# Performance work log

Measured on AMD Instinct MI355X. Metric: run time of the kernel, lower is better.

## Reference

```python
import jax, jax.numpy as jnp
import numpy as np

N, E, D_IN, D_H = 20000, 320000, 512, 512
ALPHA = 0.1
LAMBDA = 1.0

def setup_inputs() -> dict:
    key = jax.random.key(0)
    ks = jax.random.split(key, 12)
    feat = jax.random.normal(ks[0], (N, D_IN), dtype=jnp.float32)
    src = jax.random.randint(ks[1], (E,), 0, N, dtype=jnp.int32)
    dst = jax.random.randint(ks[2], (E,), 0, N, dtype=jnp.int32)
    s = 0.05
    fc_w = jax.random.normal(ks[3], (D_H, D_IN), dtype=jnp.float32) * s  # torch Linear: [out,in]
    fc_b = jax.random.normal(ks[4], (D_H,), dtype=jnp.float32) * s
    w1_1 = jax.random.normal(ks[5], (D_H, D_H), dtype=jnp.float32) * s
    w2_1 = jax.random.normal(ks[6], (D_H, D_H), dtype=jnp.float32) * s
    b_1 = jax.random.normal(ks[7], (D_H,), dtype=jnp.float32) * s
    w1_2 = jax.random.normal(ks[8], (D_H, D_H), dtype=jnp.float32) * s
    w2_2 = jax.random.normal(ks[9], (D_H, D_H), dtype=jnp.float32) * s
    b_2 = jax.random.normal(ks[10], (D_H,), dtype=jnp.float32) * s
    return {"feat": feat, "src": src, "dst": dst, "fc_w": fc_w, "fc_b": fc_b,
            "w1_1": w1_1, "w2_1": w2_1, "b_1": b_1,
            "w1_2": w1_2, "w2_2": w2_2, "b_2": b_2}


def _gcn2_layer(h, h0, src, dst, norm, w1, w2, b, layer):
    # DGL GCN2Conv (project_initial_features=False)
    beta = float(np.log(LAMBDA / layer + 1.0))
    x = h * norm                      # [N, D]
    agg = jax.ops.segment_sum(x[src], dst, num_segments=h.shape[0])  # SpMM: sum over in-neighbors
    agg = agg * norm
    f = agg * (1.0 - ALPHA)
    f0 = h0 * ALPHA
    rst = ((1.0 - beta) * f + beta * (f @ w1)
           + (1.0 - beta) * f0 + beta * (f0 @ w2) + b)
    return jax.nn.relu(rst)


def reference(feat, src, dst, fc_w, fc_b, w1_1, w2_1, b_1, w1_2, w2_2, b_2):
    n = feat.shape[0]
    h = feat @ fc_w.T + fc_b          # initial projection
    # symmetric norm from in-degrees (clamped at 1), as in DGL
    deg = jax.ops.segment_sum(jnp.ones_like(dst, dtype=h.dtype), dst, num_segments=n)
    norm = jnp.clip(deg, 1.0, None) ** -0.5
    norm = norm[:, None]
    res = _gcn2_layer(h, h, src, dst, norm, w1_1, w2_1, b_1, layer=1)
    out = _gcn2_layer(res, h, src, dst, norm, w1_2, w2_2, b_2, layer=2)
    return out
```

## Files before the change

kernel.cpp:

```cpp
#include <hip/hip_runtime.h>
#include <hip/hip_bf16.h>
#include <stdint.h>
#include <stddef.h>

typedef __bf16 bf16_t;
typedef __bf16 bf16x4 __attribute__((ext_vector_type(4)));
typedef __bf16 bf16x8 __attribute__((ext_vector_type(8)));
typedef float floatx4 __attribute__((ext_vector_type(4)));

#define NN 20000
#define EE 320000
#define DD 512
#define CAP 96
#define BETA1 0.6931471805599453f
#define BETA2 0.40546510810816444f

__device__ __forceinline__ void gload16(const bf16_t* g, bf16_t* l) {
  __builtin_amdgcn_global_load_lds((const __attribute__((address_space(1))) uint32_t*)g,
                                   (__attribute__((address_space(3))) uint32_t*)l, 16, 0, 0);
}

__global__ __launch_bounds__(256) void bucket_kernel(
    const int* __restrict__ src, const int* __restrict__ dst,
    int* __restrict__ cnt, int* __restrict__ esrc, int E) {
  int e = blockIdx.x * 256 + threadIdx.x;
  if (e < E) {
    int d = dst[e];
    int pos = atomicAdd(&cnt[d], 1);
    if (pos < CAP) esrc[d * CAP + pos] = src[e];
  }
}

#define PREP_BLOCKS 5719
__global__ __launch_bounds__(256) void prep_kernel(
    const float* __restrict__ feat, const float* __restrict__ fc_w,
    const float* __restrict__ w1_1, const float* __restrict__ w2_1,
    const float* __restrict__ w1_2, const float* __restrict__ w2_2,
    bf16_t* __restrict__ featb, bf16_t* __restrict__ bw0,
    bf16_t* __restrict__ bt1, bf16_t* __restrict__ bt2,
    int* __restrict__ cnt) {
  int b = blockIdx.x, t = threadIdx.x;
  if (b < 5128) {
    const float* in = (b < 5000) ? feat : fc_w;
    bf16_t* out = (b < 5000) ? featb : bw0;
    size_t c = (size_t)(b < 5000 ? b : b - 5000) * 256 + t;
    const float* s = in + c * 8;
    float4 v0 = *(const float4*)s, v1 = *(const float4*)(s + 4);
    bf16x8 o = {(bf16_t)v0.x, (bf16_t)v0.y, (bf16_t)v0.z, (bf16_t)v0.w,
                (bf16_t)v1.x, (bf16_t)v1.y, (bf16_t)v1.z, (bf16_t)v1.w};
    *(bf16x8*)(out + c * 8) = o;
  } else if (b < 5640) {
    int base = (b < 5384) ? 5128 : 5384;
    const float* Wa = (b < 5384) ? w1_1 : w1_2;
    const float* Wb = (b < 5384) ? w2_1 : w2_2;
    bf16_t* bt = (b < 5384) ? bt1 : bt2;
    int c = (b - base) * 256 + t;
    int n = c >> 7, kc = c & 127;
    const float* W = (kc < 64) ? Wa : Wb;
    int kcw = kc & 63;
    bf16x8 o;
#pragma unroll
    for (int e = 0; e < 8; ++e)
      o[e] = (bf16_t)W[(size_t)(kcw * 8 + e) * 512 + n];
    *(bf16x8*)(bt + (size_t)n * 1024 + kc * 8) = o;
  } else {
    int i = (b - 5640) * 256 + t;
    if (i < NN) cnt[i] = 0;
  }
}

__global__ __launch_bounds__(256) void aggregate_kernel(
    const bf16_t* __restrict__ hin, const float* __restrict__ nrm,
    const int* __restrict__ cnt, const int* __restrict__ esrc,
    bf16_t* __restrict__ Acat) {
  int node = blockIdx.x * 4 + (threadIdx.x >> 6);
  if (node >= NN) return;
  int lane = threadIdx.x & 63;
  const int* eb = esrc + (size_t)node * CAP;
  int n_e = cnt[node];
  n_e = n_e < CAP ? n_e : CAP;

  float acc[8] = {};
  bf16x8 v0 = {}, v1 = {}, v2 = {}, v3 = {}, v4 = {}, v5 = {}, v6 = {}, v7 = {};
  float ns0 = 0, ns1 = 0, ns2 = 0, ns3 = 0, ns4 = 0, ns5 = 0, ns6 = 0, ns7 = 0;

#define LOADJ(j, idx)                                                  \
  {                                                                    \
    int s = eb[idx];                                                   \
    ns##j = nrm[s];                                                    \
    v##j = *(const bf16x8*)(hin + (size_t)s * DD + lane * 8);          \
  }
#define SLOT(j, i)                                                     \
  if ((i) + (j) < n_e) {                                               \
    bf16x8 a = v##j; float na = ns##j;                                 \
    if ((i) + (j) + 8 < n_e) LOADJ(j, (i) + (j) + 8)                   \
    _Pragma("unroll")                                                  \
    for (int k = 0; k < 8; ++k) acc[k] += na * (float)a[k];            \
  }

  if (0 < n_e) LOADJ(0, 0)
  if (1 < n_e) LOADJ(1, 1)
  if (2 < n_e) LOADJ(2, 2)
  if (3 < n_e) LOADJ(3, 3)
  if (4 < n_e) LOADJ(4, 4)
  if (5 < n_e) LOADJ(5, 5)
  if (6 < n_e) LOADJ(6, 6)
  if (7 < n_e) LOADJ(7, 7)

  for (int i = 0; i < n_e; i += 8) {
    SLOT(0, i)
    SLOT(1, i)
    SLOT(2, i)
    SLOT(3, i)
    SLOT(4, i)
    SLOT(5, i)
    SLOT(6, i)
    SLOT(7, i)
  }
#undef SLOT
#undef LOADJ

  float nd = 0.9f * nrm[node];
  bf16x8 ob;
#pragma unroll
  for (int k = 0; k < 8; ++k) ob[k] = (bf16_t)(nd * acc[k]);
  *(bf16x8*)(Acat + (size_t)node * 1024 + lane * 8) = ob;
}

template <int MODE>
__global__ __launch_bounds__(256) void gemm_kernel(
    const bf16_t* __restrict__ A, const bf16_t* __restrict__ BT,
    int lda, int ldb, int K, int M,
    const float* __restrict__ bias,
    const bf16_t* __restrict__ acat_ro, float beta,
    float* __restrict__ outf, bf16_t* __restrict__ outb,
    bf16_t* __restrict__ acat2,
    const int* __restrict__ cnt, float* __restrict__ nrm) {
  __shared__ bf16_t As[2][64 * 64];
  __shared__ bf16_t Bs[2][128 * 64];

  const int bid = blockIdx.x;
  if constexpr (MODE == 0) {
    if (bid >= 1280) {
      int i = (bid - 1280) * 256 + threadIdx.x;
      if (i < NN) nrm[i] = 1.0f / sqrtf(fmaxf((float)cnt[i], 1.0f));
      return;
    }
  }
  const int mt = (bid >> 5) * 8 + (bid & 7);
  const int nt = (bid >> 3) & 3;
  const int m0 = mt * 64;
  if (m0 >= M) return;
  const int n0 = nt * 128;

  const int t = threadIdx.x;
  const int lane = t & 63;
  const int w = t >> 6;
  const int wm = w & 1, wn = w >> 1;
  const int quad = lane >> 4, m16 = lane & 15;

  const int tr = t >> 3;
  const int gc = (t & 7) ^ (tr & 7);
  int arow0 = m0 + tr;      arow0 = arow0 < M ? arow0 : M - 1;
  int arow1 = m0 + tr + 32; arow1 = arow1 < M ? arow1 : M - 1;
  const bf16_t* agp0 = A + (size_t)arow0 * lda + gc * 8;
  const bf16_t* agp1 = A + (size_t)arow1 * lda + gc * 8;
  const bf16_t* bgp0 = BT + (size_t)(n0 + tr) * ldb + gc * 8;
  const bf16_t* bgp1 = BT + (size_t)(n0 + tr + 32) * ldb + gc * 8;
  const bf16_t* bgp2 = BT + (size_t)(n0 + tr + 64) * ldb + gc * 8;
  const bf16_t* bgp3 = BT + (size_t)(n0 + tr + 96) * ldb + gc * 8;

#define STAGE(buf, ko)                              \
  gload16(agp0 + (ko), &As[buf][t * 8]);            \
  gload16(agp1 + (ko), &As[buf][(t + 256) * 8]);    \
  gload16(bgp0 + (ko), &Bs[buf][t * 8]);            \
  gload16(bgp1 + (ko), &Bs[buf][(t + 256) * 8]);    \
  gload16(bgp2 + (ko), &Bs[buf][(t + 512) * 8]);    \
  gload16(bgp3 + (ko), &Bs[buf][(t + 768) * 8]);

  floatx4 acc[2][4] = {};
  const int niter = K >> 6;

  STAGE(0, 0)

  for (int kt = 0; kt < niter; ++kt) {
    __syncthreads();
    const int b = kt & 1;
    if (kt + 1 < niter) {
      const int ko = (kt + 1) * 64;
      STAGE(b ^ 1, ko)
    }

#pragma unroll
    for (int ks = 0; ks < 2; ++ks) {
      bf16x8 af[2], bfr[4];
#pragma unroll
      for (int i = 0; i < 2; ++i) {
        int arow = wm * 32 + i * 16 + m16;
        int cc = (ks * 4 + quad) ^ (arow & 7);
        af[i] = *(const bf16x8*)(&As[b][(arow * 8 + cc) * 8]);
      }
#pragma unroll
      for (int j = 0; j < 4; ++j) {
        int brow = wn * 64 + j * 16 + m16;
        int cc = (ks * 4 + quad) ^ (brow & 7);
        bfr[j] = *(const bf16x8*)(&Bs[b][(brow * 8 + cc) * 8]);
      }
#pragma unroll
      for (int i = 0; i < 2; ++i)
#pragma unroll
        for (int j = 0; j < 4; ++j)
          acc[i][j] = __builtin_amdgcn_mfma_f32_16x16x32_bf16(af[i], bfr[j], acc[i][j], 0, 0, 0);
    }
  }
#undef STAGE

#pragma unroll
  for (int i = 0; i < 2; ++i) {
#pragma unroll
    for (int j = 0; j < 4; ++j) {
      int col = n0 + wn * 64 + j * 16 + m16;
      float bv = bias[col];
#pragma unroll
      for (int p = 0; p < 4; ++p) {
        int row = m0 + wm * 32 + i * 16 + quad * 4 + p;
        if (row < M) {
          size_t idx = (size_t)row * DD + col;
          float v = acc[i][j][p];
          if constexpr (MODE == 0) {
            float hv = v + bv;
            outb[idx] = (bf16_t)hv;
            acat2[(size_t)row * 1024 + 512 + col] = (bf16_t)(0.1f * hv);
          } else {
            float fsv = (float)acat_ro[(size_t)row * 1024 + col] +
                        (float)acat_ro[(size_t)row * 1024 + 512 + col];
            float r = (1.0f - beta) * fsv + beta * v + bv;
            r = fmaxf(r, 0.0f);
            if constexpr (MODE == 1) outb[idx] = (bf16_t)r;
            else outf[idx] = r;
          }
        }
      }
    }
  }
}

extern "C" void kernel_launch(void* const* d_in, const int* in_sizes, int n_in,
                              void* d_out, int out_size, void* d_ws, size_t ws_size,
                              hipStream_t stream) {
  const float* feat = (const float*)d_in[0];
  const int* src = (const int*)d_in[1];
  const int* dst = (const int*)d_in[2];
  const float* fc_w = (const float*)d_in[3];
  const float* fc_b = (const float*)d_in[4];
  const float* w1_1 = (const float*)d_in[5];
  const float* w2_1 = (const float*)d_in[6];
  const float* b_1  = (const float*)d_in[7];
  const float* w1_2 = (const float*)d_in[8];
  const float* w2_2 = (const float*)d_in[9];
  const float* b_2  = (const float*)d_in[10];
  float* out = (float*)d_out;

  char* ws = (char*)d_ws;
  size_t off = 0;
  auto alloc = [&](size_t bytes) {
    char* p = ws + off;
    off += (bytes + 255) & ~(size_t)255;
    return p;
  };
  const size_t NDf = (size_t)NN * DD;
  bf16_t* h_bf   = (bf16_t*)alloc(NDf * sizeof(bf16_t));
  bf16_t* res_bf = (bf16_t*)alloc(NDf * sizeof(bf16_t));
  bf16_t* featb  = (bf16_t*)alloc(NDf * sizeof(bf16_t));
  bf16_t* Acat   = (bf16_t*)alloc((size_t)NN * 1024 * sizeof(bf16_t));
  bf16_t* BW0    = (bf16_t*)alloc((size_t)512 * 512 * sizeof(bf16_t));
  bf16_t* BT1    = (bf16_t*)alloc((size_t)512 * 1024 * sizeof(bf16_t));
  bf16_t* BT2    = (bf16_t*)alloc((size_t)512 * 1024 * sizeof(bf16_t));
  int*    cnt    = (int*)alloc((size_t)NN * sizeof(int));
  float*  nrm    = (float*)alloc((size_t)NN * sizeof(float));
  int*    esrc   = (int*)alloc((size_t)NN * CAP * sizeof(int));

  prep_kernel<<<PREP_BLOCKS, 256, 0, stream>>>(feat, fc_w, w1_1, w2_1, w1_2, w2_2,
                                               featb, BW0, BT1, BT2, cnt);
  bucket_kernel<<<(EE + 255) / 256, 256, 0, stream>>>(src, dst, cnt, esrc, EE);

  gemm_kernel<0><<<1280 + 79, 256, 0, stream>>>(featb, BW0, 512, 512, 512, NN, fc_b,
                                                nullptr, 0.0f, nullptr, h_bf, Acat,
                                                cnt, nrm);

  aggregate_kernel<<<(NN + 3) / 4, 256, 0, stream>>>(h_bf, nrm, cnt, esrc, Acat);
  gemm_kernel<1><<<1280, 256, 0, stream>>>(Acat, BT1, 1024, 1024, 1024, NN, b_1,
                                           Acat, BETA1, nullptr, res_bf, nullptr,
                                           nullptr, nullptr);

  aggregate_kernel<<<(NN + 3) / 4, 256, 0, stream>>>(res_bf, nrm, cnt, esrc, Acat);
  gemm_kernel<2><<<1280, 256, 0, stream>>>(Acat, BT2, 1024, 1024, 1024, NN, b_2,
                                           Acat, BETA2, out, nullptr, nullptr,
                                           nullptr, nullptr);
}
```

Before: 360.7 us.

## Use triple-buffered K=32 LDS pipeline with explicit vmcnt waits in GEMM

Changes the GEMM mainloop from a double-buffered 64-wide K tile to a triple-buffered 32-wide K tile, with two stages in flight. Each iteration waits with s_waitcnt vmcnt(3) instead of a full __syncthreads drain, and the LDS layout and swizzle are adjusted to the narrower rows. The goal is to hide global-load latency better and keep LDS usage similar. The cost is twice as many barriers per K and less MFMA work between them.

Measured after the change: 381.4 us. 1.06x slower.

```diff
diff --git a/kernel.cpp b/kernel.cpp
--- a/kernel.cpp
+++ b/kernel.cpp
@@ -136,8 +136,8 @@
     float* __restrict__ outf, bf16_t* __restrict__ outb,
     bf16_t* __restrict__ acat2,
     const int* __restrict__ cnt, float* __restrict__ nrm) {
-  __shared__ bf16_t As[2][64 * 64];
-  __shared__ bf16_t Bs[2][128 * 64];
+  __shared__ bf16_t As[3][64 * 32];
+  __shared__ bf16_t Bs[3][128 * 32];
 
   const int bid = blockIdx.x;
   if constexpr (MODE == 0) {
@@ -159,61 +159,71 @@
   const int wm = w & 1, wn = w >> 1;
   const int quad = lane >> 4, m16 = lane & 15;
 
-  const int tr = t >> 3;
-  const int gc = (t & 7) ^ (tr & 7);
-  int arow0 = m0 + tr;      arow0 = arow0 < M ? arow0 : M - 1;
-  int arow1 = m0 + tr + 32; arow1 = arow1 < M ? arow1 : M - 1;
-  const bf16_t* agp0 = A + (size_t)arow0 * lda + gc * 8;
-  const bf16_t* agp1 = A + (size_t)arow1 * lda + gc * 8;
-  const bf16_t* bgp0 = BT + (size_t)(n0 + tr) * ldb + gc * 8;
-  const bf16_t* bgp1 = BT + (size_t)(n0 + tr + 32) * ldb + gc * 8;
-  const bf16_t* bgp2 = BT + (size_t)(n0 + tr + 64) * ldb + gc * 8;
-  const bf16_t* bgp3 = BT + (size_t)(n0 + tr + 96) * ldb + gc * 8;
+  const int hi = t >> 3;
+  const int z = (t & 7) ^ (hi & 7);
+  const int ra = hi * 2 + (z >> 2);
+  const int gc = z & 3;
+  int arow = m0 + ra; arow = arow < M ? arow : M - 1;
+  const bf16_t* agp  = A + (size_t)arow * lda + gc * 8;
+  const bf16_t* bgp0 = BT + (size_t)(n0 + ra) * ldb + gc * 8;
+  const bf16_t* bgp1 = BT + (size_t)(n0 + 64 + ra) * ldb + gc * 8;
 
 #define STAGE(buf, ko)                              \
-  gload16(agp0 + (ko), &As[buf][t * 8]);            \
-  gload16(agp1 + (ko), &As[buf][(t + 256) * 8]);    \
+  gload16(agp + (ko),  &As[buf][t * 8]);            \
   gload16(bgp0 + (ko), &Bs[buf][t * 8]);            \
-  gload16(bgp1 + (ko), &Bs[buf][(t + 256) * 8]);    \
-  gload16(bgp2 + (ko), &Bs[buf][(t + 512) * 8]);    \
-  gload16(bgp3 + (ko), &Bs[buf][(t + 768) * 8]);
+  gload16(bgp1 + (ko), &Bs[buf][(t + 256) * 8]);
+
+#define COMPUTE(b)                                                               \
+  {                                                                              \
+    bf16x8 af[2], bfr[4];                                                        \
+    _Pragma("unroll")                                                            \
+    for (int i = 0; i < 2; ++i) {                                                \
+      int ar = wm * 32 + i * 16 + m16;                                           \
+      int s8 = (((ar & 1) << 2) | quad) ^ ((ar >> 1) & 7);                       \
+      af[i] = *(const bf16x8*)(&As[b][((ar >> 1) * 8 + s8) * 8]);                \
+    }                                                                            \
+    _Pragma("unroll")                                                            \
+    for (int j = 0; j < 4; ++j) {                                                \
+      int br = wn * 64 + j * 16 + m16;                                           \
+      int s8 = (((br & 1) << 2) | quad) ^ ((br >> 1) & 7);                       \
+      bfr[j] = *(const bf16x8*)(&Bs[b][((br >> 1) * 8 + s8) * 8]);               \
+    }                                                                            \
+    _Pragma("unroll")                                                            \
+    for (int i = 0; i < 2; ++i)                                                  \
+      _Pragma("unroll")                                                          \
+      for (int j = 0; j < 4; ++j)                                                \
+        acc[i][j] = __builtin_amdgcn_mfma_f32_16x16x32_bf16(af[i], bfr[j],       \
+                                                            acc[i][j], 0, 0, 0); \
+  }
 
   floatx4 acc[2][4] = {};
-  const int niter = K >> 6;
+  const int niter = K >> 5;
 
   STAGE(0, 0)
-
-  for (int kt = 0; kt < niter; ++kt) {
-    __syncthreads();
-    const int b = kt & 1;
-    if (kt + 1 < niter) {
-      const int ko = (kt + 1) * 64;
-      STAGE(b ^ 1, ko)
+  STAGE(1, 32)
+
+  int cur = 0, nx = 2;
+  for (int kt = 0; kt < niter - 1; ++kt) {
+    asm volatile("s_waitcnt vmcnt(3)" ::: "memory");
+    asm volatile("s_waitcnt lgkmcnt(0)" ::: "memory");
+    __builtin_amdgcn_s_barrier();
+    __builtin_amdgcn_sched_barrier(0);
+    if (kt + 2 < niter) {
+      const int ko = (kt + 2) * 32;
+      STAGE(nx, ko)
     }
-
-#pragma unroll
-    for (int ks = 0; ks < 2; ++ks) {
-      bf16x8 af[2], bfr[4];
-#pragma unroll
-      for (int i = 0; i < 2; ++i) {
-        int arow = wm * 32 + i * 16 + m16;
-        int cc = (ks * 4 + quad) ^ (arow & 7);
-        af[i] = *(const bf16x8*)(&As[b][(arow * 8 + cc) * 8]);
-      }
-#pragma unroll
-      for (int j = 0; j < 4; ++j) {
-        int brow = wn * 64 + j * 16 + m16;
-        int cc = (ks * 4 + quad) ^ (brow & 7);
-        bfr[j] = *(const bf16x8*)(&Bs[b][(brow * 8 + cc) * 8]);
-      }
-#pragma unroll
-      for (int i = 0; i < 2; ++i)
-#pragma unroll
-        for (int j = 0; j < 4; ++j)
-          acc[i][j] = __builtin_amdgcn_mfma_f32_16x16x32_bf16(af[i], bfr[j], acc[i][j], 0, 0, 0);
-    }
-  }
+    COMPUTE(cur)
+    cur = (cur == 2) ? 0 : cur + 1;
+    nx = (nx == 2) ? 0 : nx + 1;
+  }
+  asm volatile("s_waitcnt vmcnt(0)" ::: "memory");
+  asm volatile("s_waitcnt lgkmcnt(0)" ::: "memory");
+  __builtin_amdgcn_s_barrier();
+  __builtin_amdgcn_sched_barrier(0);
+  COMPUTE(cur)
+
 #undef STAGE
+#undef COMPUTE
 
 #pragma unroll
   for (int i = 0; i < 2; ++i) {
```

## Store unscaled h once in Acat and aggregate two nodes per wavefront

Applied to the files above, without the earlier changes.

The first GEMM now writes the unscaled projection h only into the second half of Acat, instead of writing both a separate h buffer and a 0.1-scaled copy. The 0.1 factor is folded into the W2 weight conversion and the epilogue, and the first aggregation reads h from Acat with a stride of 1024. The aggregation kernel also handles two destination nodes per wavefront, each with 4 in-flight loads, so more independent gathers are outstanding at once. The aim is to cut a full N×512 bf16 write and shorten gather latency, at the cost of strided reads and uneven work when the two nodes have different degrees.

After: 370.5 us. 2.7% more time.

```diff
diff --git a/kernel.cpp b/kernel.cpp
--- a/kernel.cpp
+++ b/kernel.cpp
@@ -57,11 +57,12 @@
     int c = (b - base) * 256 + t;
     int n = c >> 7, kc = c & 127;
     const float* W = (kc < 64) ? Wa : Wb;
+    const float sc = (kc < 64) ? 1.0f : 0.1f;
     int kcw = kc & 63;
     bf16x8 o;
 #pragma unroll
     for (int e = 0; e < 8; ++e)
-      o[e] = (bf16_t)W[(size_t)(kcw * 8 + e) * 512 + n];
+      o[e] = (bf16_t)(sc * W[(size_t)(kcw * 8 + e) * 512 + n]);
     *(bf16x8*)(bt + (size_t)n * 1024 + kc * 8) = o;
   } else {
     int i = (b - 5640) * 256 + t;
@@ -70,61 +71,86 @@
 }
 
 __global__ __launch_bounds__(256) void aggregate_kernel(
-    const bf16_t* __restrict__ hin, const float* __restrict__ nrm,
+    const bf16_t* __restrict__ hin, int hstride, const float* __restrict__ nrm,
     const int* __restrict__ cnt, const int* __restrict__ esrc,
     bf16_t* __restrict__ Acat) {
-  int node = blockIdx.x * 4 + (threadIdx.x >> 6);
-  if (node >= NN) return;
+  int nodeA = blockIdx.x * 8 + (threadIdx.x >> 6) * 2;
+  int nodeB = nodeA + 1;
+  if (nodeA >= NN) return;
   int lane = threadIdx.x & 63;
-  const int* eb = esrc + (size_t)node * CAP;
-  int n_e = cnt[node];
-  n_e = n_e < CAP ? n_e : CAP;
-
-  float acc[8] = {};
-  bf16x8 v0 = {}, v1 = {}, v2 = {}, v3 = {}, v4 = {}, v5 = {}, v6 = {}, v7 = {};
-  float ns0 = 0, ns1 = 0, ns2 = 0, ns3 = 0, ns4 = 0, ns5 = 0, ns6 = 0, ns7 = 0;
-
-#define LOADJ(j, idx)                                                  \
-  {                                                                    \
-    int s = eb[idx];                                                   \
-    ns##j = nrm[s];                                                    \
-    v##j = *(const bf16x8*)(hin + (size_t)s * DD + lane * 8);          \
-  }
-#define SLOT(j, i)                                                     \
-  if ((i) + (j) < n_e) {                                               \
-    bf16x8 a = v##j; float na = ns##j;                                 \
-    if ((i) + (j) + 8 < n_e) LOADJ(j, (i) + (j) + 8)                   \
-    _Pragma("unroll")                                                  \
-    for (int k = 0; k < 8; ++k) acc[k] += na * (float)a[k];            \
-  }
-
-  if (0 < n_e) LOADJ(0, 0)
-  if (1 < n_e) LOADJ(1, 1)
-  if (2 < n_e) LOADJ(2, 2)
-  if (3 < n_e) LOADJ(3, 3)
-  if (4 < n_e) LOADJ(4, 4)
-  if (5 < n_e) LOADJ(5, 5)
-  if (6 < n_e) LOADJ(6, 6)
-  if (7 < n_e) LOADJ(7, 7)
-
-  for (int i = 0; i < n_e; i += 8) {
-    SLOT(0, i)
-    SLOT(1, i)
-    SLOT(2, i)
-    SLOT(3, i)
-    SLOT(4, i)
-    SLOT(5, i)
-    SLOT(6, i)
-    SLOT(7, i)
-  }
-#undef SLOT
-#undef LOADJ
-
-  float nd = 0.9f * nrm[node];
-  bf16x8 ob;
-#pragma unroll
-  for (int k = 0; k < 8; ++k) ob[k] = (bf16_t)(nd * acc[k]);
-  *(bf16x8*)(Acat + (size_t)node * 1024 + lane * 8) = ob;
+  const int* ebA = esrc + (size_t)nodeA * CAP;
+  const int* ebB = esrc + (size_t)nodeB * CAP;
+  int nA = cnt[nodeA]; nA = nA < CAP ? nA : CAP;
+  int nB = cnt[nodeB]; nB = nB < CAP ? nB : CAP;
+  int nmax = nA > nB ? nA : nB;
+
+  float accA[8] = {}, accB[8] = {};
+  bf16x8 va0 = {}, va1 = {}, va2 = {}, va3 = {};
+  bf16x8 vb0 = {}, vb1 = {}, vb2 = {}, vb3 = {};
+  float sa0 = 0, sa1 = 0, sa2 = 0, sa3 = 0;
+  float sb0 = 0, sb1 = 0, sb2 = 0, sb3 = 0;
+
+#define LDA(j, idx)                                                      \
+  {                                                                      \
+    int s = ebA[idx];                                                    \
+    sa##j = nrm[s];                                                      \
+    va##j = *(const bf16x8*)(hin + (size_t)s * hstride + lane * 8);      \
+  }
+#define LDB(j, idx)                                                      \
+  {                                                                      \
+    int s = ebB[idx];                                                    \
+    sb##j = nrm[s];                                                      \
+    vb##j = *(const bf16x8*)(hin + (size_t)s * hstride + lane * 8);      \
+  }
+#define SLA(j, i)                                                        \
+  if ((i) + (j) < nA) {                                                  \
+    bf16x8 a = va##j; float na = sa##j;                                  \
+    if ((i) + (j) + 4 < nA) LDA(j, (i) + (j) + 4)                        \
+    _Pragma("unroll")                                                    \
+    for (int k = 0; k < 8; ++k) accA[k] += na * (float)a[k];             \
+  }
+#define SLB(j, i)                                                        \
+  if ((i) + (j) < nB) {                                                  \
+    bf16x8 a = vb##j; float na = sb##j;                                  \
+    if ((i) + (j) + 4 < nB) LDB(j, (i) + (j) + 4)                        \
+    _Pragma("unroll")                                                    \
+    for (int k = 0; k < 8; ++k) accB[k] += na * (float)a[k];             \
+  }
+
+  if (0 < nA) LDA(0, 0)
+  if (0 < nB) LDB(0, 0)
+  if (1 < nA) LDA(1, 1)
+  if (1 < nB) LDB(1, 1)
+  if (2 < nA) LDA(2, 2)
+  if (2 < nB) LDB(2, 2)
+  if (3 < nA) LDA(3, 3)
+  if (3 < nB) LDB(3, 3)
+
+  for (int i = 0; i < nmax; i += 4) {
+    SLA(0, i)
+    SLB(0, i)
+    SLA(1, i)
+    SLB(1, i)
+    SLA(2, i)
+    SLB(2, i)
+    SLA(3, i)
+    SLB(3, i)
+  }
+#undef SLA
+#undef SLB
+#undef LDA
+#undef LDB
+
+  float ndA = 0.9f * nrm[nodeA];
+  float ndB = 0.9f * nrm[nodeB];
+  bf16x8 oA, oB;
+#pragma unroll
+  for (int k = 0; k < 8; ++k) {
+    oA[k] = (bf16_t)(ndA * accA[k]);
+    oB[k] = (bf16_t)(ndB * accB[k]);
+  }
+  *(bf16x8*)(Acat + (size_t)nodeA * 1024 + lane * 8) = oA;
+  *(bf16x8*)(Acat + (size_t)nodeB * 1024 + lane * 8) = oB;
 }
 
 template <int MODE>
@@ -225,15 +251,13 @@
       for (int p = 0; p < 4; ++p) {
         int row = m0 + wm * 32 + i * 16 + quad * 4 + p;
         if (row < M) {
-          size_t idx = (size_t)row * DD + col;
           float v = acc[i][j][p];
           if constexpr (MODE == 0) {
-            float hv = v + bv;
-            outb[idx] = (bf16_t)hv;
-            acat2[(size_t)row * 1024 + 512 + col] = (bf16_t)(0.1f * hv);
+            acat2[(size_t)row * 1024 + 512 + col] = (bf16_t)(v + bv);
           } else {
+            size_t idx = (size_t)row * DD + col;
             float fsv = (float)acat_ro[(size_t)row * 1024 + col] +
-                        (float)acat_ro[(size_t)row * 1024 + 512 + col];
+                        0.1f * (float)acat_ro[(size_t)row * 1024 + 512 + col];
             float r = (1.0f - beta) * fsv + beta * v + bv;
             r = fmaxf(r, 0.0f);
             if constexpr (MODE == 1) outb[idx] = (bf16_t)r;
@@ -269,7 +293,6 @@
     return p;
   };
   const size_t NDf = (size_t)NN * DD;
-  bf16_t* h_bf   = (bf16_t*)alloc(NDf * sizeof(bf16_t));
   bf16_t* res_bf = (bf16_t*)alloc(NDf * sizeof(bf16_t));
   bf16_t* featb  = (bf16_t*)alloc(NDf * sizeof(bf16_t));
   bf16_t* Acat   = (bf16_t*)alloc((size_t)NN * 1024 * sizeof(bf16_t));
@@ -285,15 +308,15 @@
   bucket_kernel<<<(EE + 255) / 256, 256, 0, stream>>>(src, dst, cnt, esrc, EE);
 
   gemm_kernel<0><<<1280 + 79, 256, 0, stream>>>(featb, BW0, 512, 512, 512, NN, fc_b,
-                                                nullptr, 0.0f, nullptr, h_bf, Acat,
+                                                nullptr, 0.0f, nullptr, nullptr, Acat,
                                                 cnt, nrm);
 
-  aggregate_kernel<<<(NN + 3) / 4, 256, 0, stream>>>(h_bf, nrm, cnt, esrc, Acat);
+  aggregate_kernel<<<NN / 8, 256, 0, stream>>>(Acat + 512, 1024, nrm, cnt, esrc, Acat);
   gemm_kernel<1><<<1280, 256, 0, stream>>>(Acat, BT1, 1024, 1024, 1024, NN, b_1,
                                            Acat, BETA1, nullptr, res_bf, nullptr,
                                            nullptr, nullptr);
 
-  aggregate_kernel<<<(NN + 3) / 4, 256, 0, stream>>>(res_bf, nrm, cnt, esrc, Acat);
+  aggregate_kernel<<<NN / 8, 256, 0, stream>>>(res_bf, 512, nrm, cnt, esrc, Acat);
   gemm_kernel<2><<<1280, 256, 0, stream>>>(Acat, BT2, 1024, 1024, 1024, NN, b_2,
                                            Acat, BETA2, out, nullptr, nullptr,
                                            nullptr, nullptr);
```

## Pre-scale features by source norm and pipeline aggregation gathers through LDS

Applied to the files above, without the earlier changes.

The GEMM epilogues now write features already multiplied by the source-node norm (computed inline from degree counts), so the aggregation no longer loads a per-edge norm and the separate norm array and pass are removed. The 0.1 alpha factor moves into the W2 weights and the epilogue. The aggregation kernel is rewritten to load edge indices four at a time and gather neighbor rows asynchronously into a double-buffered LDS ring using global_load_lds with explicit vmcnt waits. To keep the fixed-size chunk index loads safe, the prep kernel zero-fills the edge bucket buffer, which adds extra write traffic.

New measurement: 342.6 us. 1.05x faster.

```diff
diff --git a/kernel.cpp b/kernel.cpp
--- a/kernel.cpp
+++ b/kernel.cpp
@@ -31,14 +31,14 @@
   }
 }
 
-#define PREP_BLOCKS 5719
+#define PREP_BLOCKS 7594
 __global__ __launch_bounds__(256) void prep_kernel(
     const float* __restrict__ feat, const float* __restrict__ fc_w,
     const float* __restrict__ w1_1, const float* __restrict__ w2_1,
     const float* __restrict__ w1_2, const float* __restrict__ w2_2,
     bf16_t* __restrict__ featb, bf16_t* __restrict__ bw0,
     bf16_t* __restrict__ bt1, bf16_t* __restrict__ bt2,
-    int* __restrict__ cnt) {
+    int* __restrict__ cnt, int* __restrict__ esrc) {
   int b = blockIdx.x, t = threadIdx.x;
   if (b < 5128) {
     const float* in = (b < 5000) ? feat : fc_w;
@@ -57,70 +57,89 @@
     int c = (b - base) * 256 + t;
     int n = c >> 7, kc = c & 127;
     const float* W = (kc < 64) ? Wa : Wb;
+    const float sc = (kc < 64) ? 1.0f : 0.1f;
     int kcw = kc & 63;
     bf16x8 o;
 #pragma unroll
     for (int e = 0; e < 8; ++e)
-      o[e] = (bf16_t)W[(size_t)(kcw * 8 + e) * 512 + n];
+      o[e] = (bf16_t)(sc * W[(size_t)(kcw * 8 + e) * 512 + n]);
     *(bf16x8*)(bt + (size_t)n * 1024 + kc * 8) = o;
-  } else {
+  } else if (b < 5719) {
     int i = (b - 5640) * 256 + t;
     if (i < NN) cnt[i] = 0;
+  } else {
+    int i = (b - 5719) * 256 + t;
+    ((int4*)esrc)[i] = make_int4(0, 0, 0, 0);
   }
 }
 
 __global__ __launch_bounds__(256) void aggregate_kernel(
-    const bf16_t* __restrict__ hin, const float* __restrict__ nrm,
-    const int* __restrict__ cnt, const int* __restrict__ esrc,
-    bf16_t* __restrict__ Acat) {
-  int node = blockIdx.x * 4 + (threadIdx.x >> 6);
-  if (node >= NN) return;
-  int lane = threadIdx.x & 63;
+    const bf16_t* __restrict__ hs, const int* __restrict__ cnt,
+    const int* __restrict__ esrc, bf16_t* __restrict__ Acat) {
+  __shared__ bf16_t ring[4][2][4][512];
+  const int w = threadIdx.x >> 6;
+  const int lane = threadIdx.x & 63;
+  const int node = blockIdx.x * 4 + w;
   const int* eb = esrc + (size_t)node * CAP;
-  int n_e = cnt[node];
-  n_e = n_e < CAP ? n_e : CAP;
+  int ncnt = cnt[node];
+  int n_e = ncnt < CAP ? ncnt : CAP;
+  float nd = 0.9f * rsqrtf(fmaxf((float)ncnt, 1.0f));
+  int nchunks = (n_e + 3) >> 2;
 
   float acc[8] = {};
-  bf16x8 v0 = {}, v1 = {}, v2 = {}, v3 = {}, v4 = {}, v5 = {}, v6 = {}, v7 = {};
-  float ns0 = 0, ns1 = 0, ns2 = 0, ns3 = 0, ns4 = 0, ns5 = 0, ns6 = 0, ns7 = 0;
-
-#define LOADJ(j, idx)                                                  \
-  {                                                                    \
-    int s = eb[idx];                                                   \
-    ns##j = nrm[s];                                                    \
-    v##j = *(const bf16x8*)(hin + (size_t)s * DD + lane * 8);          \
-  }
-#define SLOT(j, i)                                                     \
-  if ((i) + (j) < n_e) {                                               \
-    bf16x8 a = v##j; float na = ns##j;                                 \
-    if ((i) + (j) + 8 < n_e) LOADJ(j, (i) + (j) + 8)                   \
-    _Pragma("unroll")                                                  \
-    for (int k = 0; k < 8; ++k) acc[k] += na * (float)a[k];            \
-  }
-
-  if (0 < n_e) LOADJ(0, 0)
-  if (1 < n_e) LOADJ(1, 1)
-  if (2 < n_e) LOADJ(2, 2)
-  if (3 < n_e) LOADJ(3, 3)
-  if (4 < n_e) LOADJ(4, 4)
-  if (5 < n_e) LOADJ(5, 5)
-  if (6 < n_e) LOADJ(6, 6)
-  if (7 < n_e) LOADJ(7, 7)
-
-  for (int i = 0; i < n_e; i += 8) {
-    SLOT(0, i)
-    SLOT(1, i)
-    SLOT(2, i)
-    SLOT(3, i)
-    SLOT(4, i)
-    SLOT(5, i)
-    SLOT(6, i)
-    SLOT(7, i)
-  }
-#undef SLOT
-#undef LOADJ
-
-  float nd = 0.9f * nrm[node];
+  bf16_t* r0base = &ring[w][0][0][lane * 8];
+  bf16_t* r1base = &ring[w][1][0][lane * 8];
+
+  int4 icur, inext;
+
+  asm volatile("s_waitcnt vmcnt(0)" ::: "memory");
+  __builtin_amdgcn_sched_barrier(0);
+  icur = *(const int4*)(eb);
+  asm volatile("s_waitcnt vmcnt(0)" ::: "memory");
+  __builtin_amdgcn_sched_barrier(0);
+  inext = *(const int4*)(eb + 4);
+  gload16(hs + (size_t)icur.x * DD + lane * 8, r0base);
+  gload16(hs + (size_t)icur.y * DD + lane * 8, r0base + 512);
+  gload16(hs + (size_t)icur.z * DD + lane * 8, r0base + 1024);
+  gload16(hs + (size_t)icur.w * DD + lane * 8, r0base + 1536);
+
+  for (int c = 0; c < nchunks; ++c) {
+    asm volatile("s_waitcnt vmcnt(4)" ::: "memory");
+    __builtin_amdgcn_sched_barrier(0);
+    int4 iuse = inext;
+    int off2 = (c + 2) * 4; off2 = off2 > CAP - 4 ? CAP - 4 : off2;
+    inext = *(const int4*)(eb + off2);
+    bf16_t* rbn = ((c + 1) & 1) ? r1base : r0base;
+    gload16(hs + (size_t)iuse.x * DD + lane * 8, rbn);
+    gload16(hs + (size_t)iuse.y * DD + lane * 8, rbn + 512);
+    gload16(hs + (size_t)iuse.z * DD + lane * 8, rbn + 1024);
+    gload16(hs + (size_t)iuse.w * DD + lane * 8, rbn + 1536);
+    asm volatile("s_waitcnt vmcnt(5)" ::: "memory");
+    __builtin_amdgcn_sched_barrier(0);
+    bf16_t* rb = (c & 1) ? r1base : r0base;
+    bf16x8 v0 = *(const bf16x8*)(rb);
+    bf16x8 v1 = *(const bf16x8*)(rb + 512);
+    bf16x8 v2 = *(const bf16x8*)(rb + 1024);
+    bf16x8 v3 = *(const bf16x8*)(rb + 1536);
+    int e0 = c * 4;
+    if (e0 < n_e) {
+#pragma unroll
+      for (int k = 0; k < 8; ++k) acc[k] += (float)v0[k];
+    }
+    if (e0 + 1 < n_e) {
+#pragma unroll
+      for (int k = 0; k < 8; ++k) acc[k] += (float)v1[k];
+    }
+    if (e0 + 2 < n_e) {
+#pragma unroll
+      for (int k = 0; k < 8; ++k) acc[k] += (float)v2[k];
+    }
+    if (e0 + 3 < n_e) {
+#pragma unroll
+      for (int k = 0; k < 8; ++k) acc[k] += (float)v3[k];
+    }
+  }
+
   bf16x8 ob;
 #pragma unroll
   for (int k = 0; k < 8; ++k) ob[k] = (bf16_t)(nd * acc[k]);
@@ -135,18 +154,11 @@
     const bf16_t* __restrict__ acat_ro, float beta,
     float* __restrict__ outf, bf16_t* __restrict__ outb,
     bf16_t* __restrict__ acat2,
-    const int* __restrict__ cnt, float* __restrict__ nrm) {
+    const int* __restrict__ cnt) {
   __shared__ bf16_t As[2][64 * 64];
   __shared__ bf16_t Bs[2][128 * 64];
 
   const int bid = blockIdx.x;
-  if constexpr (MODE == 0) {
-    if (bid >= 1280) {
-      int i = (bid - 1280) * 256 + threadIdx.x;
-      if (i < NN) nrm[i] = 1.0f / sqrtf(fmaxf((float)cnt[i], 1.0f));
-      return;
-    }
-  }
   const int mt = (bid >> 5) * 8 + (bid & 7);
   const int nt = (bid >> 3) & 3;
   const int m0 = mt * 64;
@@ -215,6 +227,18 @@
   }
 #undef STAGE
 
+  float rsv[2][4];
+  if constexpr (MODE != 2) {
+#pragma unroll
+    for (int i = 0; i < 2; ++i)
+#pragma unroll
+      for (int p = 0; p < 4; ++p) {
+        int row = m0 + wm * 32 + i * 16 + quad * 4 + p;
+        int rowc = row < M ? row : M - 1;
+        rsv[i][p] = rsqrtf(fmaxf((float)cnt[rowc], 1.0f));
+      }
+  }
+
 #pragma unroll
   for (int i = 0; i < 2; ++i) {
 #pragma unroll
@@ -225,18 +249,18 @@
       for (int p = 0; p < 4; ++p) {
         int row = m0 + wm * 32 + i * 16 + quad * 4 + p;
         if (row < M) {
-          size_t idx = (size_t)row * DD + col;
           float v = acc[i][j][p];
           if constexpr (MODE == 0) {
             float hv = v + bv;
-            outb[idx] = (bf16_t)hv;
-            acat2[(size_t)row * 1024 + 512 + col] = (bf16_t)(0.1f * hv);
+            acat2[(size_t)row * 1024 + 512 + col] = (bf16_t)hv;
+            outb[(size_t)row * DD + col] = (bf16_t)(rsv[i][p] * hv);
           } else {
+            size_t idx = (size_t)row * DD + col;
             float fsv = (float)acat_ro[(size_t)row * 1024 + col] +
-                        (float)acat_ro[(size_t)row * 1024 + 512 + col];
+                        0.1f * (float)acat_ro[(size_t)row * 1024 + 512 + col];
             float r = (1.0f - beta) * fsv + beta * v + bv;
             r = fmaxf(r, 0.0f);
-            if constexpr (MODE == 1) outb[idx] = (bf16_t)r;
+            if constexpr (MODE == 1) outb[idx] = (bf16_t)(rsv[i][p] * r);
             else outf[idx] = r;
           }
         }
@@ -269,32 +293,28 @@
     return p;
   };
   const size_t NDf = (size_t)NN * DD;
-  bf16_t* h_bf   = (bf16_t*)alloc(NDf * sizeof(bf16_t));
   bf16_t* res_bf = (bf16_t*)alloc(NDf * sizeof(bf16_t));
   bf16_t* featb  = (bf16_t*)alloc(NDf * sizeof(bf16_t));
+  bf16_t* hs     = (bf16_t*)alloc(NDf * sizeof(bf16_t));
   bf16_t* Acat   = (bf16_t*)alloc((size_t)NN * 1024 * sizeof(bf16_t));
   bf16_t* BW0    = (bf16_t*)alloc((size_t)512 * 512 * sizeof(bf16_t));
   bf16_t* BT1    = (bf16_t*)alloc((size_t)512 * 1024 * sizeof(bf16_t));
   bf16_t* BT2    = (bf16_t*)alloc((size_t)512 * 1024 * sizeof(bf16_t));
   int*    cnt    = (int*)alloc((size_t)NN * sizeof(int));
-  float*  nrm    = (float*)alloc((size_t)NN * sizeof(float));
-  int*    esrc   = (int*)alloc((size_t)NN * CAP * sizeof(int));
+  int*    esrc   = (int*)alloc(((size_t)NN * CAP + 64) * sizeof(int));
 
   prep_kernel<<<PREP_BLOCKS, 256, 0, stream>>>(feat, fc_w, w1_1, w2_1, w1_2, w2_2,
-                                               featb, BW0, BT1, BT2, cnt);
+                                               featb, BW0, BT1, BT2, cnt, esrc);
   bucket_kernel<<<(EE + 255) / 256, 256, 0, stream>>>(src, dst, cnt, esrc, EE);
 
-  gemm_kernel<0><<<1280 + 79, 256, 0, stream>>>(featb, BW0, 512, 512, 512, NN, fc_b,
-                                                nullptr, 0.0f, nullptr, h_bf, Acat,
-                                                cnt, nrm);
-
-  aggregate_kernel<<<(NN + 3) / 4, 256, 0, stream>>>(h_bf, nrm, cnt, esrc, Acat);
+  gemm_kernel<0><<<1280, 256, 0, stream>>>(featb, BW0, 512, 512, 512, NN, fc_b,
+                                           nullptr, 0.0f, nullptr, hs, Acat, cnt);
+
+  aggregate_kernel<<<NN / 4, 256, 0, stream>>>(hs, cnt, esrc, Acat);
   gemm_kernel<1><<<1280, 256, 0, stream>>>(Acat, BT1, 1024, 1024, 1024, NN, b_1,
-                                           Acat, BETA1, nullptr, res_bf, nullptr,
-                                           nullptr, nullptr);
-
-  aggregate_kernel<<<(NN + 3) / 4, 256, 0, stream>>>(res_bf, nrm, cnt, esrc, Acat);
+                                           Acat, BETA1, nullptr, res_bf, nullptr, cnt);
+
+  aggregate_kernel<<<NN / 4, 256, 0, stream>>>(res_bf, cnt, esrc, Acat);
   gemm_kernel<2><<<1280, 256, 0, stream>>>(Acat, BT2, 1024, 1024, 1024, NN, b_2,
-                                           Acat, BETA2, out, nullptr, nullptr,
-                                           nullptr, nullptr);
-}
+                                           Acat, BETA2, out, nullptr, nullptr, nullptr);
+}
```
